# Performance work log

Measured on AMD Instinct MI355X. Metric: run time of the kernel, lower is better.

Reference implementation:

```python
import jax, jax.numpy as jnp
import numpy as np

N_EMBD = 1024
N_HEAD = 16
HEAD_DIM = N_EMBD // N_HEAD

def setup_inputs() -> dict:
    key = jax.random.key(0)
    ks = jax.random.split(key, 9)
    B, T, C = 2, 2048, N_EMBD
    s = 1.0 / np.sqrt(C)
    x = jax.random.normal(ks[0], (B, T, C), dtype=jnp.float32)
    Wk = jax.random.normal(ks[1], (C, C), dtype=jnp.float32) * s
    bk = jnp.zeros((C,), dtype=jnp.float32)
    Wq = jax.random.normal(ks[2], (C, C), dtype=jnp.float32) * s
    bq = jnp.zeros((C,), dtype=jnp.float32)
    Wv = jax.random.normal(ks[3], (C, C), dtype=jnp.float32) * s
    bv = jnp.zeros((C,), dtype=jnp.float32)
    Wp = jax.random.normal(ks[4], (C, C), dtype=jnp.float32) * s
    bp = jnp.zeros((C,), dtype=jnp.float32)
    return {"x": x, "Wq": Wq, "bq": bq, "Wk": Wk, "bk": bk, "Wv": Wv, "bv": bv, "Wp": Wp, "bp": bp}

def reference(x, Wq, bq, Wk, bk, Wv, bv, Wp, bp):
    B, T, C = x.shape
    H, D = N_HEAD, HEAD_DIM
    # QKV projections (torch Linear: x @ W.T + b; here W is stored as (in,out))
    q = (x @ Wq + bq).reshape(B, T, H, D).transpose(0, 2, 1, 3)  # [B,H,T,D]
    k = (x @ Wk + bk).reshape(B, T, H, D).transpose(0, 2, 1, 3)
    v = (x @ Wv + bv).reshape(B, T, H, D).transpose(0, 2, 1, 3)
    att = jnp.einsum('bhtd,bhsd->bhts', q, k) / jnp.sqrt(jnp.float32(D))
    causal = jnp.tril(jnp.ones((T, T), dtype=bool))
    att = jnp.where(causal, att, jnp.float32(-jnp.inf))
    att = jax.nn.softmax(att, axis=-1)
    y = jnp.einsum('bhts,bhsd->bhtd', att, v)  # [B,H,T,D]
    y = y.transpose(0, 2, 1, 3).reshape(B, T, C)
    return y @ Wp + bp
```

## Files before the change

kernel.cpp:

```cpp
#include <hip/hip_runtime.h>
#include <cstdint>

typedef __attribute__((ext_vector_type(4))) short s16x4;
typedef __attribute__((ext_vector_type(8))) short s16x8;
typedef __attribute__((ext_vector_type(4))) float f32x4;
typedef __attribute__((ext_vector_type(16))) float f32x16;

#define L2E 1.44269504088896340736f

__device__ __forceinline__ short f2bf(float f) {
  union { float f; unsigned u; } v; v.f = f;
  unsigned r = (v.u + 0x7fffu + ((v.u >> 16) & 1u)) >> 16;
  return (short)r;
}

__device__ __forceinline__ float xhalf_f(float x) {
  union { float f; unsigned u; } a; a.f = x;
  auto r = __builtin_amdgcn_permlane32_swap(a.u, a.u, false, false);
  union { unsigned u; float f; } b;
  b.u = (threadIdx.x & 32) ? r[0] : r[1];
  return b.f;
}

typedef const __attribute__((address_space(1))) unsigned int* gas_p;
typedef __attribute__((address_space(3))) unsigned int* las_p;
__device__ __forceinline__ void stage16(const void* g, void* l) {
  __builtin_amdgcn_global_load_lds((gas_p)(uintptr_t)g,
                                   (las_p)(unsigned int)(uintptr_t)l, 16, 0, 0);
}

__global__ __launch_bounds__(256) void prepass(const float* __restrict__ W0,
                                               const float* __restrict__ W1,
                                               const float* __restrict__ W2,
                                               const float* __restrict__ W3,
                                               short* __restrict__ wdst,
                                               const float* __restrict__ x,
                                               short* __restrict__ xb) {
  const int z = blockIdx.z;
  const int t = threadIdx.x;
  if (z >= 4) {
    int i = ((z - 4) * 256 + blockIdx.y * 16 + blockIdx.x) * 256 + t;
    const f32x4* p = (const f32x4*)x + (size_t)i * 2;
    f32x4 a = p[0], b = p[1];
    s16x8 o;
    o[0] = f2bf(a[0]); o[1] = f2bf(a[1]); o[2] = f2bf(a[2]); o[3] = f2bf(a[3]);
    o[4] = f2bf(b[0]); o[5] = f2bf(b[1]); o[6] = f2bf(b[2]); o[7] = f2bf(b[3]);
    *((s16x8*)xb + i) = o;
    return;
  }
  __shared__ float tile[64][65];
  const float* in = (z == 0) ? W0 : (z == 1) ? W1 : (z == 2) ? W2 : W3;
  short* out = wdst + (size_t)z * 1048576;
  const int bi = blockIdx.y, bj = blockIdx.x;
  const int c = t & 63, r0 = t >> 6;
#pragma unroll
  for (int i = 0; i < 16; i++) {
    int r = r0 + i * 4;
    tile[r][c] = in[(size_t)(bi * 64 + r) * 1024 + bj * 64 + c];
  }
  __syncthreads();
#pragma unroll
  for (int i = 0; i < 16; i++) {
    int r = r0 + i * 4;
    out[(size_t)(bj * 64 + r) * 1024 + bi * 64 + c] = f2bf(tile[c][r]);
  }
}

template <int EPI, int BM>
__global__ __launch_bounds__(BM * 2) void gemm_bt(
    const short* __restrict__ A, const short* __restrict__ B, int N, int K,
    const float* __restrict__ b0, const float* __restrict__ b1,
    const float* __restrict__ b2, short* __restrict__ o0, short* __restrict__ o1,
    short* __restrict__ o2, float* __restrict__ ofp) {
  constexpr int T = BM * 2;
  constexpr int AR = BM * 8 / T;
  constexpr int BR = 128 * 8 / T;
  constexpr int LOADS = AR + BR;
  constexpr int BUFB = (BM + 128) * 64;
  __shared__ short L[3 * BUFB];
  const int tid = threadIdx.x;
  const int lane = tid & 63;
  const int wave = tid >> 6;
  const int wr = wave >> 1, wc = wave & 1;
  const int l15 = lane & 15, l4 = lane >> 4;
  const int id = blockIdx.x + gridDim.x * blockIdx.y;
  const int cpx = gridDim.x >> 3;
  const int xcd = id & 7, sub = id >> 3;
  const int m0 = (sub / cpx) * BM;
  const int n0 = (xcd * cpx + sub % cpx) * 128;
  f32x4 acc[4][4];
#pragma unroll
  for (int i = 0; i < 4; i++)
#pragma unroll
    for (int j = 0; j < 4; j++) acc[i][j] = (f32x4){0.f, 0.f, 0.f, 0.f};

  const int lq = tid & 3, lr = tid >> 2;
  int soffA[AR], goffA[AR];
#pragma unroll
  for (int i = 0; i < AR; i++) {
    const int flat = i * (T / 4) + lr;
    const int p = flat / BM, r = flat % BM;
    soffA[i] = p * BM * 32 + r * 32 + lq * 8;
    goffA[i] = r * K + p * 32 + lq * 8;
  }
  int soffB[BR], goffB[BR];
#pragma unroll
  for (int j = 0; j < BR; j++) {
    const int flat = j * (T / 4) + lr;
    const int p = flat >> 7, r = flat & 127;
    soffB[j] = BM * 64 + p * 4096 + r * 32 + lq * 8;
    goffB[j] = r * K + p * 32 + lq * 8;
  }

  const short* Asrc = A + (size_t)m0 * K;
  const short* Bsrc = B + (size_t)n0 * K;
  short* bufC = L;
  short* bufN = L + BUFB;
  short* bufS = L + 2 * BUFB;

#define GSTAGE(BUF)                                                            \
  {                                                                            \
    _Pragma("unroll") for (int i_ = 0; i_ < AR; i_++)                          \
        stage16(Asrc + goffA[i_], (BUF) + soffA[i_]);                          \
    _Pragma("unroll") for (int j_ = 0; j_ < BR; j_++)                          \
        stage16(Bsrc + goffB[j_], (BUF) + soffB[j_]);                          \
    Asrc += 64; Bsrc += 64;                                                    \
  }

  GSTAGE(bufC)
  GSTAGE(bufN)
  asm volatile("s_waitcnt vmcnt(%0)" ::"i"(LOADS) : "memory");
  __builtin_amdgcn_s_barrier();
  __builtin_amdgcn_sched_barrier(0);

  const int NK = K >> 6;
  for (int kt = 0; kt < NK; kt++) {
    if (kt + 2 < NK) GSTAGE(bufS)
#pragma unroll
    for (int ks = 0; ks < 2; ks++) {
      s16x8 af[4], bfr[4];
#pragma unroll
      for (int i = 0; i < 4; i++) {
        af[i] = *(const s16x8*)(bufC + ks * BM * 32 + (wr * 64 + i * 16 + l15) * 32 + l4 * 8);
        bfr[i] = *(const s16x8*)(bufC + BM * 64 + ks * 4096 + (wc * 64 + i * 16 + l15) * 32 + l4 * 8);
      }
#pragma unroll
      for (int mi = 0; mi < 4; mi++)
#pragma unroll
        for (int ni = 0; ni < 4; ni++)
          acc[mi][ni] = __builtin_amdgcn_mfma_f32_16x16x32_bf16(af[mi], bfr[ni],
                                                                acc[mi][ni], 0, 0, 0);
    }
    if (kt + 1 < NK) {
      if (kt + 2 < NK) {
        asm volatile("s_waitcnt vmcnt(%0)" ::"i"(LOADS) : "memory");
      } else {
        asm volatile("s_waitcnt vmcnt(0)" ::: "memory");
      }
      __builtin_amdgcn_s_barrier();
      __builtin_amdgcn_sched_barrier(0);
      short* t_ = bufC; bufC = bufN; bufN = bufS; bufS = t_;
    }
  }
#undef GSTAGE

#pragma unroll
  for (int ni = 0; ni < 4; ni++) {
    const int col = n0 + wc * 64 + ni * 16 + l15;
    if (EPI == 1) {
      const float bias = b0[col];
#pragma unroll
      for (int mi = 0; mi < 4; mi++)
#pragma unroll
        for (int r = 0; r < 4; r++) {
          int row = m0 + wr * 64 + mi * 16 + l4 * 4 + r;
          ofp[(size_t)row * N + col] = acc[mi][ni][r] + bias;
        }
    } else {
      const float* bp; short* dst; int c1; int isV = 0; float scl = 1.0f;
      if (col < 1024) { bp = b0; dst = o0; c1 = col; scl = 0.125f * L2E; }
      else if (col < 2048) { bp = b1; dst = o1; c1 = col - 1024; }
      else { bp = b2; dst = o2; c1 = col - 2048; isV = 1; }
      const float bias = bp[c1];
      const int h = c1 >> 6, d = c1 & 63;
      if (isV) {
#pragma unroll
        for (int mi = 0; mi < 4; mi++) {
          int t0 = m0 + wr * 64 + mi * 16 + l4 * 4;
          int bb = t0 >> 11, t = t0 & 2047;
          s16x4 ov;
#pragma unroll
          for (int r = 0; r < 4; r++) ov[r] = f2bf(acc[mi][ni][r] + bias);
          *(s16x4*)(dst + (size_t)((bb * 16 + h) * 64 + d) * 2048 + t) = ov;
        }
      } else {
#pragma unroll
        for (int mi = 0; mi < 4; mi++)
#pragma unroll
          for (int r = 0; r < 4; r++) {
            int row = m0 + wr * 64 + mi * 16 + l4 * 4 + r;
            int bb = row >> 11, t = row & 2047;
            float v = (acc[mi][ni][r] + bias) * scl;
            dst[(size_t)((bb * 16 + h) * 2048 + t) * 64 + d] = f2bf(v);
          }
      }
    }
  }
}

__global__ __launch_bounds__(128) void attn_v8(const short* __restrict__ Q,
                                               const short* __restrict__ K,
                                               const short* __restrict__ Vt,
                                               short* __restrict__ Y) {
  __shared__ short Ks[2][64 * 64];
  __shared__ short Vs[3][64 * 64];
  const int bh = blockIdx.x;
  const int y = blockIdx.y;
  const int g = y >> 3, r_ = y & 7;
  const int qbase = (g << 3) | ((g & 1) ? (7 - r_) : r_);
  const int qt = (qbase + ((bh & 3) << 3)) & 31;
  const int tid = threadIdx.x, lane = tid & 63, wave = tid >> 6;
  const int q31 = lane & 31, hi = lane >> 5;
  const short* Qp = Q + (size_t)bh * 2048 * 64;
  const short* Kp = K + (size_t)bh * 2048 * 64;
  const short* Vp = Vt + (size_t)bh * 64 * 2048;
  const int qrow = qt * 64 + wave * 32 + q31;
  const int nt = qt + 1;
  const int cx = q31 & 7;

  s16x8 qf[4];
#pragma unroll
  for (int s = 0; s < 4; s++)
    qf[s] = *(const s16x8*)(Qp + (size_t)qrow * 64 + s * 16 + hi * 8);

  f32x16 accA, accB, Z;
#pragma unroll
  for (int i = 0; i < 16; i++) { accA[i] = 0.f; accB[i] = 0.f; Z[i] = 0.f; }
  float l = 0.f;

  const int srow = tid >> 3, sch = tid & 7;
  int sdst[4], koff[4], voff[4];
#pragma unroll
  for (int i = 0; i < 4; i++) {
    const int r = srow + i * 16;
    const int sc = sch ^ (r & 7);
    sdst[i] = r * 64 + sch * 8;
    koff[i] = r * 64 + sc * 8;
    voff[i] = r * 2048 + sc * 8;
  }
  const short* kst = Kp;
  const short* vst = Vp;
  int rd0[4];
#pragma unroll
  for (int s = 0; s < 4; s++) rd0[s] = q31 * 64 + (((2 * s + hi) ^ cx) << 3);

  short* kA = &Ks[0][0]; short* kB = &Ks[1][0];
  short* vP = &Vs[2][0]; short* vC = &Vs[0][0]; short* vN = &Vs[1][0];

#pragma unroll
  for (int i = 0; i < 4; i++) {
    stage16(kst + koff[i], kA + sdst[i]);
    stage16(vst + voff[i], vC + sdst[i]);
  }
  kst += 4096; vst += 64;

#define STAGE_NEXT(COND)                                                       \
  if (COND) {                                                                  \
    _Pragma("unroll") for (int i_ = 0; i_ < 4; i_++) {                         \
      stage16(kst + koff[i_], kB + sdst[i_]);                                  \
      stage16(vst + voff[i_], vN + sdst[i_]);                                  \
    }                                                                          \
    kst += 4096; vst += 64;                                                    \
  }

#define QK(S0, S1)                                                             \
  {                                                                            \
    s16x8 kf0_[4], kf1_[4];                                                    \
    _Pragma("unroll") for (int s_ = 0; s_ < 4; s_++) {                         \
      kf0_[s_] = *(const s16x8*)(kA + rd0[s_]);                                \
      kf1_[s_] = *(const s16x8*)(kA + rd0[s_] + 2048);                         \
    }                                                                          \
    __builtin_amdgcn_s_setprio(1);                                             \
    S0 = __builtin_amdgcn_mfma_f32_32x32x16_bf16(kf0_[0], qf[0], Z, 0, 0, 0);  \
    S1 = __builtin_amdgcn_mfma_f32_32x32x16_bf16(kf1_[0], qf[0], Z, 0, 0, 0);  \
    _Pragma("unroll") for (int s_ = 1; s_ < 4; s_++) {                         \
      S0 = __builtin_amdgcn_mfma_f32_32x32x16_bf16(kf0_[s_], qf[s_], S0, 0, 0, 0); \
      S1 = __builtin_amdgcn_mfma_f32_32x32x16_bf16(kf1_[s_], qf[s_], S1, 0, 0, 0); \
    }                                                                          \
    __builtin_amdgcn_s_setprio(0);                                             \
  }

#define SMPV_BODY(S0, S1)                                                      \
  {                                                                            \
    float rsum_ = 0.f;                                                         \
    _Pragma("unroll") for (int r2_ = 0; r2_ < 16; r2_++) {                     \
      float p_ = __builtin_amdgcn_exp2f(S0[r2_]);                              \
      S0[r2_] = p_; rsum_ += p_;                                               \
    }                                                                          \
    _Pragma("unroll") for (int r2_ = 0; r2_ < 16; r2_++) {                     \
      float p_ = __builtin_amdgcn_exp2f(S1[r2_]);                              \
      S1[r2_] = p_; rsum_ += p_;                                               \
    }                                                                          \
    l += rsum_;                                                                \
    unsigned pk0_[8], pk1_[8];                                                 \
    _Pragma("unroll") for (int j_ = 0; j_ < 8; j_++) {                         \
      unsigned u_;                                                             \
      float a0_ = S0[2 * j_], a1_ = S0[2 * j_ + 1];                            \
      asm("v_cvt_pk_bf16_f32 %0, %1, %2" : "=v"(u_) : "v"(a0_), "v"(a1_));     \
      pk0_[j_] = u_;                                                           \
      float b0_ = S1[2 * j_], b1_ = S1[2 * j_ + 1];                            \
      asm("v_cvt_pk_bf16_f32 %0, %1, %2" : "=v"(u_) : "v"(b0_), "v"(b1_));     \
      pk1_[j_] = u_;                                                           \
    }                                                                          \
    _Pragma("unroll") for (int s_ = 0; s_ < 4; s_++) {                         \
      const unsigned* pk_ = (s_ < 2) ? pk0_ : pk1_;                            \
      const int b_ = 4 * (s_ & 1);                                             \
      auto rA_ = __builtin_amdgcn_permlane32_swap(pk_[b_ + 0], pk_[b_ + 2], false, false); \
      auto rB_ = __builtin_amdgcn_permlane32_swap(pk_[b_ + 1], pk_[b_ + 3], false, false); \
      union { unsigned u[4]; s16x8 v; } fr_;                                   \
      fr_.u[0] = rA_[0]; fr_.u[1] = rB_[0]; fr_.u[2] = rA_[1]; fr_.u[3] = rB_[1]; \
      s16x8 vf0_ = *(const s16x8*)(vP + rd0[s_]);                              \
      s16x8 vf1_ = *(const s16x8*)(vP + rd0[s_] + 2048);                       \
      __builtin_amdgcn_s_setprio(1);                                           \
      accA = __builtin_amdgcn_mfma_f32_32x32x16_bf16(vf0_, fr_.v, accA, 0, 0, 0); \
      accB = __builtin_amdgcn_mfma_f32_32x32x16_bf16(vf1_, fr_.v, accB, 0, 0, 0); \
      __builtin_amdgcn_s_setprio(0);                                           \
    }                                                                          \
  }

#define SMPV_MASK(S0, S1)                                                      \
  {                                                                            \
    const int k0_ = (nt - 1) * 64;                                             \
    _Pragma("unroll") for (int r2_ = 0; r2_ < 16; r2_++) {                     \
      int kvr_ = k0_ + (r2_ & 3) + 8 * (r2_ >> 2) + 4 * hi;                    \
      if (kvr_ > qrow) S0[r2_] = -__builtin_inff();                            \
      if (kvr_ + 32 > qrow) S1[r2_] = -__builtin_inff();                       \
    }                                                                          \
    SMPV_BODY(S0, S1)                                                          \
  }

#define ROT()                                                                  \
  {                                                                            \
    short* t_ = kA; kA = kB; kB = t_;                                          \
    t_ = vP; vP = vC; vC = vN; vN = t_;                                        \
  }

  f32x16 sA0, sA1, sB0, sB1;
  __syncthreads();
  STAGE_NEXT(nt > 1)
  QK(sA0, sA1)
  ROT()
  int t = 1;
  for (; t + 1 < nt; t += 2) {
    __syncthreads();
    STAGE_NEXT(t + 1 < nt)
    QK(sB0, sB1)
    SMPV_BODY(sA0, sA1)
    ROT()
    __syncthreads();
    STAGE_NEXT(t + 2 < nt)
    QK(sA0, sA1)
    SMPV_BODY(sB0, sB1)
    ROT()
  }
  if (t < nt) {
    __syncthreads();
    QK(sB0, sB1)
    SMPV_BODY(sA0, sA1)
    ROT()
    SMPV_MASK(sB0, sB1)
  } else {
    SMPV_MASK(sA0, sA1)
  }
#undef STAGE_NEXT
#undef QK
#undef SMPV_BODY
#undef SMPV_MASK
#undef ROT

  const int b_ = bh >> 4, h_ = bh & 15;
  const float lt = l + xhalf_f(l);
  const float invl = 1.f / lt;
  const size_t base = ((size_t)b_ * 2048 + qrow) * 1024 + h_ * 64;
#pragma unroll
  for (int gg = 0; gg < 4; gg++) {
    s16x4 o0, o1;
#pragma unroll
    for (int e = 0; e < 4; e++) {
      o0[e] = f2bf(accA[4 * gg + e] * invl);
      o1[e] = f2bf(accB[4 * gg + e] * invl);
    }
    *(s16x4*)(Y + base + 8 * gg + 4 * hi) = o0;
    *(s16x4*)(Y + base + 32 + 8 * gg + 4 * hi) = o1;
  }
}

extern "C" void kernel_launch(void* const* d_in, const int* in_sizes, int n_in,
                              void* d_out, int out_size, void* d_ws, size_t ws_size,
                              hipStream_t stream) {
  const float* x = (const float*)d_in[0];
  const float* Wq = (const float*)d_in[1];
  const float* bq = (const float*)d_in[2];
  const float* Wk = (const float*)d_in[3];
  const float* bk = (const float*)d_in[4];
  const float* Wv = (const float*)d_in[5];
  const float* bv = (const float*)d_in[6];
  const float* Wp = (const float*)d_in[7];
  const float* bp = (const float*)d_in[8];
  float* out = (float*)d_out;
  char* ws = (char*)d_ws;

  short* xb    = (short*)(ws + 0);
  short* WqkvT = (short*)(ws + 8388608);
  short* WpT   = (short*)(ws + 14680064);
  short* Qb    = (short*)(ws + 16777216);
  short* Kb    = (short*)(ws + 25165824);
  short* Vtb   = (short*)(ws + 33554432);
  short* Yb    = xb;

  prepass<<<dim3(16, 16, 12), 256, 0, stream>>>(Wq, Wk, Wv, Wp, WqkvT, x, xb);
  gemm_bt<0, 256><<<dim3(24, 16), 512, 0, stream>>>(xb, WqkvT, 3072, 1024, bq, bk,
                                                    bv, Qb, Kb, Vtb, nullptr);
  attn_v8<<<dim3(32, 32), 128, 0, stream>>>(Qb, Kb, Vtb, Yb);
  gemm_bt<1, 128><<<dim3(8, 32), 256, 0, stream>>>(Yb, WpT, 1024, 1024, bp, nullptr,
                                                   nullptr, nullptr, nullptr,
                                                   nullptr, out);
}
```

Baseline: 110.3 us.

## Simplify GEMM to double-buffered BK=32 pipeline and shrink output-projection tile

```diff
diff --git a/kernel.cpp b/kernel.cpp
--- a/kernel.cpp
+++ b/kernel.cpp
@@ -73,11 +73,10 @@
     const float* __restrict__ b2, short* __restrict__ o0, short* __restrict__ o1,
     short* __restrict__ o2, float* __restrict__ ofp) {
   constexpr int T = BM * 2;
-  constexpr int AR = BM * 8 / T;
-  constexpr int BR = 128 * 8 / T;
-  constexpr int LOADS = AR + BR;
-  constexpr int BUFB = (BM + 128) * 64;
-  __shared__ short L[3 * BUFB];
+  constexpr int AR = 2;
+  constexpr int BR = 512 / T;
+  constexpr int BUFB = (BM + 128) * 32;
+  __shared__ short L[2 * BUFB];
   const int tid = threadIdx.x;
   const int lane = tid & 63;
   const int wave = tid >> 6;
@@ -98,25 +97,22 @@
   int soffA[AR], goffA[AR];
 #pragma unroll
   for (int i = 0; i < AR; i++) {
-    const int flat = i * (T / 4) + lr;
-    const int p = flat / BM, r = flat % BM;
-    soffA[i] = p * BM * 32 + r * 32 + lq * 8;
-    goffA[i] = r * K + p * 32 + lq * 8;
+    const int r = i * (T / 4) + lr;
+    soffA[i] = r * 32 + lq * 8;
+    goffA[i] = r * K + lq * 8;
   }
   int soffB[BR], goffB[BR];
 #pragma unroll
   for (int j = 0; j < BR; j++) {
-    const int flat = j * (T / 4) + lr;
-    const int p = flat >> 7, r = flat & 127;
-    soffB[j] = BM * 64 + p * 4096 + r * 32 + lq * 8;
-    goffB[j] = r * K + p * 32 + lq * 8;
+    const int r = j * (T / 4) + lr;
+    soffB[j] = BM * 32 + r * 32 + lq * 8;
+    goffB[j] = r * K + lq * 8;
   }
 
   const short* Asrc = A + (size_t)m0 * K;
   const short* Bsrc = B + (size_t)n0 * K;
   short* bufC = L;
   short* bufN = L + BUFB;
-  short* bufS = L + 2 * BUFB;
 
 #define GSTAGE(BUF)                                                            \
   {                                                                            \
@@ -124,43 +120,27 @@
         stage16(Asrc + goffA[i_], (BUF) + soffA[i_]);                          \
     _Pragma("unroll") for (int j_ = 0; j_ < BR; j_++)                          \
         stage16(Bsrc + goffB[j_], (BUF) + soffB[j_]);                          \
-    Asrc += 64; Bsrc += 64;                                                    \
+    Asrc += 32; Bsrc += 32;                                                    \
   }
 
   GSTAGE(bufC)
-  GSTAGE(bufN)
-  asm volatile("s_waitcnt vmcnt(%0)" ::"i"(LOADS) : "memory");
-  __builtin_amdgcn_s_barrier();
-  __builtin_amdgcn_sched_barrier(0);
-
-  const int NK = K >> 6;
+  const int NK = K >> 5;
   for (int kt = 0; kt < NK; kt++) {
-    if (kt + 2 < NK) GSTAGE(bufS)
-#pragma unroll
-    for (int ks = 0; ks < 2; ks++) {
-      s16x8 af[4], bfr[4];
-#pragma unroll
-      for (int i = 0; i < 4; i++) {
-        af[i] = *(const s16x8*)(bufC + ks * BM * 32 + (wr * 64 + i * 16 + l15) * 32 + l4 * 8);
-        bfr[i] = *(const s16x8*)(bufC + BM * 64 + ks * 4096 + (wc * 64 + i * 16 + l15) * 32 + l4 * 8);
-      }
-#pragma unroll
-      for (int mi = 0; mi < 4; mi++)
-#pragma unroll
-        for (int ni = 0; ni < 4; ni++)
-          acc[mi][ni] = __builtin_amdgcn_mfma_f32_16x16x32_bf16(af[mi], bfr[ni],
-                                                                acc[mi][ni], 0, 0, 0);
+    __syncthreads();
+    if (kt + 1 < NK) GSTAGE(bufN)
+    s16x8 af[4], bfr[4];
+#pragma unroll
+    for (int i = 0; i < 4; i++) {
+      af[i] = *(const s16x8*)(bufC + (wr * 64 + i * 16 + l15) * 32 + l4 * 8);
+      bfr[i] = *(const s16x8*)(bufC + BM * 32 + (wc * 64 + i * 16 + l15) * 32 + l4 * 8);
     }
-    if (kt + 1 < NK) {
-      if (kt + 2 < NK) {
-        asm volatile("s_waitcnt vmcnt(%0)" ::"i"(LOADS) : "memory");
-      } else {
-        asm volatile("s_waitcnt vmcnt(0)" ::: "memory");
-      }
-      __builtin_amdgcn_s_barrier();
-      __builtin_amdgcn_sched_barrier(0);
-      short* t_ = bufC; bufC = bufN; bufN = bufS; bufS = t_;
-    }
+#pragma unroll
+    for (int mi = 0; mi < 4; mi++)
+#pragma unroll
+      for (int ni = 0; ni < 4; ni++)
+        acc[mi][ni] = __builtin_amdgcn_mfma_f32_16x16x32_bf16(af[mi], bfr[ni],
+                                                              acc[mi][ni], 0, 0, 0);
+    short* t_ = bufC; bufC = bufN; bufN = t_;
   }
 #undef GSTAGE
 
@@ -422,7 +402,7 @@
   gemm_bt<0, 256><<<dim3(24, 16), 512, 0, stream>>>(xb, WqkvT, 3072, 1024, bq, bk,
                                                     bv, Qb, Kb, Vtb, nullptr);
   attn_v8<<<dim3(32, 32), 128, 0, stream>>>(Qb, Kb, Vtb, Yb);
-  gemm_bt<1, 128><<<dim3(8, 32), 256, 0, stream>>>(Yb, WpT, 1024, 1024, bp, nullptr,
-                                                   nullptr, nullptr, nullptr,
-                                                   nullptr, out);
-}
+  gemm_bt<1, 64><<<dim3(8, 64), 128, 0, stream>>>(Yb, WpT, 1024, 1024, bp, nullptr,
+                                                  nullptr, nullptr, nullptr,
+                                                  nullptr, out);
+}
```

Result: faster. 105.0 us (-4.8%).
